# Performance work log

Hardware: AMD Instinct MI355X
Metric: run time of the kernel (lower is better)

Reference implementation:

```python
import jax, jax.numpy as jnp
import numpy as np

# ---- static configuration (matches init_kwargs) ----
B = 256              # graph pairs -> 2B graphs total (query/corpus interleaved)
N_PER_GRAPH = 24     # nodes per graph
N_MAX = 32           # max node set size (transport plan side)
E_PER_GRAPH = 200    # edges per graph
E_MAX = 256          # max_edge_set_size
D_EDGE = 256         # edge_feature_dim
D_SINK = 256         # sinkhorn_feature_dim
TEMPERATURE = 0.1
NUM_SINKHORN_ITERS = 20
NOISE_FACTOR = 0.0   # deterministic sinkhorn
CONSISTENCY_WEIGHT = 1.0


def setup_inputs() -> dict:
    rng = np.random.RandomState(0)
    num_graphs = 2 * B
    node_offset = np.arange(num_graphs) * N_PER_GRAPH
    graph_idx = np.repeat(np.arange(num_graphs), N_PER_GRAPH)
    # edges are grouped by graph (standard batched-graph layout)
    from_local = rng.randint(0, N_PER_GRAPH, size=(num_graphs, E_PER_GRAPH))
    to_local = rng.randint(0, N_PER_GRAPH, size=(num_graphs, E_PER_GRAPH))
    from_idx = (from_local + node_offset[:, None]).reshape(-1)
    to_idx = (to_local + node_offset[:, None]).reshape(-1)
    total_edges = num_graphs * E_PER_GRAPH

    key = jax.random.key(0)
    k = jax.random.split(key, 4)
    return {
        "edge_features_enc": jax.random.normal(k[0], (total_edges, D_EDGE), jnp.float32),
        "node_transport_plan": jax.random.uniform(k[1], (B, N_MAX, N_MAX), jnp.float32),
        "W1": jax.random.normal(k[2], (D_EDGE, D_SINK), jnp.float32) / np.sqrt(D_EDGE).astype(np.float32),
        "b1": jnp.zeros((D_SINK,), jnp.float32),
        "W2": jax.random.normal(k[3], (D_SINK, D_SINK), jnp.float32) / np.sqrt(D_SINK).astype(np.float32),
        "b2": jnp.zeros((D_SINK,), jnp.float32),
        "from_idx": jnp.asarray(from_idx, jnp.int32),
        "to_idx": jnp.asarray(to_idx, jnp.int32),
        "graph_idx": jnp.asarray(graph_idx, jnp.int32),
        "query_sizes": jnp.full((B,), N_PER_GRAPH, jnp.int32),
        "corpus_sizes": jnp.full((B,), N_PER_GRAPH, jnp.int32),
    }


def reference(edge_features_enc, node_transport_plan, W1, b1, W2, b2,
              from_idx, to_idx, graph_idx, query_sizes, corpus_sizes):
    num_graphs = 2 * B
    total_edges = from_idx.shape[0]

    # --- get_paired_edge_counts / split_and_stack ---
    g_edge = graph_idx[from_idx]                                   # graph id per edge
    edge_counts = jax.ops.segment_sum(jnp.ones_like(g_edge), g_edge, num_segments=num_graphs)
    edge_offset = jnp.cumsum(edge_counts) - edge_counts            # exclusive prefix
    rank = jnp.arange(total_edges, dtype=jnp.int32) - edge_offset[g_edge]

    stacked = jnp.zeros((num_graphs, E_MAX, D_EDGE), edge_features_enc.dtype)
    stacked = stacked.at[g_edge, rank].set(edge_features_enc)      # [2B, E_MAX, D]
    q_feat, c_feat = stacked[0::2], stacked[1::2]

    # --- sinkhorn_feature_layers (Linear-ReLU-Linear) + size mask ---
    def mlp(x):
        return jax.nn.relu(x @ W1 + b1) @ W2 + b2
    q_feat, c_feat = mlp(q_feat), mlp(c_feat)
    pos = jnp.arange(E_MAX)
    q_feat = q_feat * (pos[None, :] < query_sizes[:, None]).astype(q_feat.dtype)[..., None]
    c_feat = c_feat * (pos[None, :] < corpus_sizes[:, None]).astype(c_feat.dtype)[..., None]

    # --- kronecker_product_on_nodes: local endpoint ids, pad slots -> zero row N_MAX ---
    node_counts = jax.ops.segment_sum(jnp.ones_like(graph_idx), graph_idx, num_segments=num_graphs)
    node_offset = jnp.cumsum(node_counts) - node_counts
    pad = jnp.full((num_graphs, E_MAX), N_MAX, jnp.int32)
    f_loc = pad.at[g_edge, rank].set(from_idx - node_offset[g_edge])
    t_loc = pad.at[g_edge, rank].set(to_idx - node_offset[g_edge])
    fq, fc = f_loc[0::2], f_loc[1::2]
    tq, tc = t_loc[0::2], t_loc[1::2]

    T = jnp.pad(node_transport_plan, ((0, 0), (0, 1), (0, 1)))     # zero row/col for pads
    b = jnp.arange(B)[:, None, None]
    straight = T[b, fq[:, :, None], fc[:, None, :]] * T[b, tq[:, :, None], tc[:, None, :]]
    cross = T[b, fq[:, :, None], tc[:, None, :]] * T[b, tq[:, :, None], fc[:, None, :]]

    # --- sinkhorn_iters (log domain, noise_factor=0) ---
    log_alpha = (straight + cross) / TEMPERATURE                   # [B, E_MAX, E_MAX]
    def step(la, _):
        la = la - jax.nn.logsumexp(la, axis=2, keepdims=True)
        la = la - jax.nn.logsumexp(la, axis=1, keepdims=True)
        return la, None
    log_alpha, _ = jax.lax.scan(step, log_alpha, None, length=NUM_SINKHORN_ITERS)
    plan = jnp.exp(log_alpha)

    # --- feature_alignment_score: -sum(relu(q - P c)) per pair ---
    score = -jax.nn.relu(q_feat - plan @ c_feat).sum(axis=(1, 2))
    return CONSISTENCY_WEIGHT * score
```

## Files before the change

kernel.cpp:

```cpp
#include <hip/hip_runtime.h>

typedef unsigned short ushort_t;
typedef unsigned int uint_t;

typedef float f32x4_t __attribute__((ext_vector_type(4)));
typedef short s16x8_t __attribute__((ext_vector_type(8)));

#define NB   256
#define NG   512
#define NPG  24
#define NMAXI 32
#define EPG  200
#define DD   256
#define L2E_OVER_T 14.426950408889634f

__device__ __forceinline__ ushort_t f2bf(float f) {
    uint_t u = __float_as_uint(f);
    u += 0x7FFFu + ((u >> 16) & 1u);
    return (ushort_t)(u >> 16);
}
__device__ __forceinline__ float bfhi(uint_t u) { return __uint_as_float(u & 0xFFFF0000u); }
__device__ __forceinline__ float bflo(uint_t u) { return __uint_as_float(u << 16); }

__device__ __forceinline__ float frcp(float x) {
#if __has_builtin(__builtin_amdgcn_rcpf)
    return __builtin_amdgcn_rcpf(x);
#else
    return 1.0f / x;
#endif
}

__global__ __launch_bounds__(256) void prep_w(const float* __restrict__ W1,
                                              const float* __restrict__ W2,
                                              ushort_t* __restrict__ W1T,
                                              ushort_t* __restrict__ W2T)
{
    __shared__ float tile[2][4 * 256];
    const int t = threadIdx.x;
    const int k0 = blockIdx.x * 4;
    #pragma unroll
    for (int i = t; i < 4 * 256; i += 256) {
        tile[0][i] = W1[k0 * 256 + i];
        tile[1][i] = W2[k0 * 256 + i];
    }
    __syncthreads();
    const int n = t;
    #pragma unroll
    for (int m = 0; m < 2; ++m) {
        uint_t p0 = (uint_t)f2bf(tile[m][0 * 256 + n]) | ((uint_t)f2bf(tile[m][1 * 256 + n]) << 16);
        uint_t p1 = (uint_t)f2bf(tile[m][2 * 256 + n]) | ((uint_t)f2bf(tile[m][3 * 256 + n]) << 16);
        ushort_t* dst = (m ? W2T : W1T) + n * 256 + k0;
        uint2 pk; pk.x = p0; pk.y = p1;
        *(uint2*)dst = pk;
    }
}

__global__ __launch_bounds__(256) void mlp_kernel(
    const float* __restrict__ X, const ushort_t* __restrict__ W1T,
    const ushort_t* __restrict__ W2T, const float* __restrict__ b1,
    const float* __restrict__ b2, float* __restrict__ Y)
{
    __shared__ ushort_t sA[64 * 272];
    const int t = threadIdx.x;
    const int blk = blockIdx.x;
    const int lane = t & 63;
    const int w = t >> 6;
    const int quad = lane >> 4;
    const int mrow = lane & 15;

    {
        int r = t >> 2;
        int ch = (t & 3) * 64;
        int rho = blk * 64 + r;
        int g = rho / NPG;
        int e = rho - g * NPG;
        const float* src = X + ((size_t)(g * EPG + e)) * DD + ch;
        ushort_t* dst = &sA[r * 272 + ch];
        #pragma unroll
        for (int i = 0; i < 8; ++i) {
            float4 v0 = *(const float4*)(src + i * 8);
            float4 v1 = *(const float4*)(src + i * 8 + 4);
            uint4 pk;
            pk.x = (uint_t)f2bf(v0.x) | ((uint_t)f2bf(v0.y) << 16);
            pk.y = (uint_t)f2bf(v0.z) | ((uint_t)f2bf(v0.w) << 16);
            pk.z = (uint_t)f2bf(v1.x) | ((uint_t)f2bf(v1.y) << 16);
            pk.w = (uint_t)f2bf(v1.z) | ((uint_t)f2bf(v1.w) << 16);
            *(uint4*)(dst + i * 8) = pk;
        }
    }
    __syncthreads();

    f32x4_t acc[16];
    #pragma unroll
    for (int i = 0; i < 16; ++i) acc[i] = (f32x4_t){0.f, 0.f, 0.f, 0.f};

    #pragma unroll
    for (int k0 = 0; k0 < 256; k0 += 32) {
        s16x8_t a[4], bb[4];
        #pragma unroll
        for (int mt = 0; mt < 4; ++mt)
            a[mt] = *(const s16x8_t*)&sA[(mt * 16 + mrow) * 272 + k0 + quad * 8];
        #pragma unroll
        for (int nt = 0; nt < 4; ++nt)
            bb[nt] = *(const s16x8_t*)(W1T + (size_t)(64 * w + nt * 16 + mrow) * 256 + k0 + quad * 8);
        #pragma unroll
        for (int mt = 0; mt < 4; ++mt) {
            #pragma unroll
            for (int nt = 0; nt < 4; ++nt)
                acc[mt * 4 + nt] = __builtin_amdgcn_mfma_f32_16x16x32_bf16(
                    a[mt], bb[nt], acc[mt * 4 + nt], 0, 0, 0);
        }
    }
    __syncthreads();

    #pragma unroll
    for (int nt = 0; nt < 4; ++nt) {
        int col = 64 * w + nt * 16 + mrow;
        float bias = b1[col];
        #pragma unroll
        for (int mt = 0; mt < 4; ++mt) {
            f32x4_t v = acc[mt * 4 + nt];
            #pragma unroll
            for (int reg = 0; reg < 4; ++reg) {
                int row = mt * 16 + quad * 4 + reg;
                sA[row * 272 + col] = f2bf(fmaxf(v[reg] + bias, 0.f));
            }
        }
    }
    __syncthreads();

    #pragma unroll
    for (int i = 0; i < 16; ++i) acc[i] = (f32x4_t){0.f, 0.f, 0.f, 0.f};

    #pragma unroll
    for (int k0 = 0; k0 < 256; k0 += 32) {
        s16x8_t a[4], bb[4];
        #pragma unroll
        for (int mt = 0; mt < 4; ++mt)
            a[mt] = *(const s16x8_t*)&sA[(mt * 16 + mrow) * 272 + k0 + quad * 8];
        #pragma unroll
        for (int nt = 0; nt < 4; ++nt)
            bb[nt] = *(const s16x8_t*)(W2T + (size_t)(64 * w + nt * 16 + mrow) * 256 + k0 + quad * 8);
        #pragma unroll
        for (int mt = 0; mt < 4; ++mt) {
            #pragma unroll
            for (int nt = 0; nt < 4; ++nt)
                acc[mt * 4 + nt] = __builtin_amdgcn_mfma_f32_16x16x32_bf16(
                    a[mt], bb[nt], acc[mt * 4 + nt], 0, 0, 0);
        }
    }

    #pragma unroll
    for (int nt = 0; nt < 4; ++nt) {
        int col = 64 * w + nt * 16 + mrow;
        float bias = b2[col];
        #pragma unroll
        for (int mt = 0; mt < 4; ++mt) {
            f32x4_t v = acc[mt * 4 + nt];
            #pragma unroll
            for (int reg = 0; reg < 4; ++reg) {
                int row = blk * 64 + mt * 16 + quad * 4 + reg;
                Y[(size_t)row * 256 + col] = v[reg] + bias;
            }
        }
    }
}

__global__ __launch_bounds__(1024) void sink_kernel(
    const float* __restrict__ Tplan, const int* __restrict__ from_idx,
    const int* __restrict__ to_idx, const int* __restrict__ qsz,
    const int* __restrict__ csz, const float* __restrict__ qcf,
    float* __restrict__ out)
{
    const int b = blockIdx.x;
    const int t = threadIdx.x;
    const int R = t >> 4;
    const int C = t & 15;
    const int w = t >> 6;

    __shared__ __align__(16) char ovl[56320];
    __shared__ float ru_s[260];
    __shared__ float rv_p[320];
    __shared__ float wsum[16];

    float* Tl = (float*)ovl;
    int* fq = (int*)(ovl + 4368);
    int* tq = (int*)(ovl + 5392);
    int* fc = (int*)(ovl + 6416);
    int* tc = (int*)(ovl + 7440);
    float* Vp = (float*)ovl;
    float* plan_s = (float*)ovl;
    float* cf_s   = (float*)(ovl + 25600);

    for (int i = t; i < 33 * 33; i += 1024) Tl[i] = 0.f;
    if (t < 320) rv_p[t] = 1.0f;
    if (t < 256) {
        int gq = 2 * b, gc = 2 * b + 1;
        int a = NMAXI, bb = NMAXI, c = NMAXI, d = NMAXI;
        if (t < EPG) {
            a  = from_idx[gq * EPG + t] - gq * NPG;
            bb = to_idx  [gq * EPG + t] - gq * NPG;
            c  = from_idx[gc * EPG + t] - gc * NPG;
            d  = to_idx  [gc * EPG + t] - gc * NPG;
        }
        fq[t] = a; tq[t] = bb; fc[t] = c; tc[t] = d;
    }
    __syncthreads();
    {
        int i = t >> 5, j = t & 31;
        Tl[i * 33 + j] = Tplan[((size_t)b << 10) + t];
    }
    __syncthreads();

    uint_t Kp[4][8];
    {
        int fcl[16], tcl[16];
        #pragma unroll
        for (int o = 0; o < 16; ++o) { fcl[o] = fc[16 * C + o]; tcl[o] = tc[16 * C + o]; }
        #pragma unroll
        for (int i = 0; i < 4; ++i) {
            const float* T1 = &Tl[fq[4 * R + i] * 33];
            const float* T2 = &Tl[tq[4 * R + i] * 33];
            #pragma unroll
            for (int u = 0; u < 8; ++u) {
                int f0 = fcl[2 * u], t0 = tcl[2 * u];
                int f1 = fcl[2 * u + 1], t1 = tcl[2 * u + 1];
                float la0 = T1[f0] * T2[t0] + T1[t0] * T2[f0];
                float la1 = T1[f1] * T2[t1] + T1[t1] * T2[f1];
                Kp[i][u] = (uint_t)f2bf(exp2f(la0 * L2E_OVER_T))
                         | ((uint_t)f2bf(exp2f(la1 * L2E_OVER_T)) << 16);
            }
        }
    }

    for (int it = 0; it < 20; ++it) {
        {
            float4 rv0 = *(const float4*)&rv_p[20 * C + 0];
            float4 rv1 = *(const float4*)&rv_p[20 * C + 4];
            float4 rv2 = *(const float4*)&rv_p[20 * C + 8];
            float4 rv3 = *(const float4*)&rv_p[20 * C + 12];
            float pr[4];
            #pragma unroll
            for (int i = 0; i < 4; ++i) {
                float a0 = bflo(Kp[i][0]) * rv0.x + bfhi(Kp[i][0]) * rv0.y;
                float a1 = bflo(Kp[i][1]) * rv0.z + bfhi(Kp[i][1]) * rv0.w;
                float a2 = bflo(Kp[i][2]) * rv1.x + bfhi(Kp[i][2]) * rv1.y;
                float a3 = bflo(Kp[i][3]) * rv1.z + bfhi(Kp[i][3]) * rv1.w;
                a0 += bflo(Kp[i][4]) * rv2.x + bfhi(Kp[i][4]) * rv2.y;
                a1 += bflo(Kp[i][5]) * rv2.z + bfhi(Kp[i][5]) * rv2.w;
                a2 += bflo(Kp[i][6]) * rv3.x + bfhi(Kp[i][6]) * rv3.y;
                a3 += bflo(Kp[i][7]) * rv3.z + bfhi(Kp[i][7]) * rv3.w;
                pr[i] = (a0 + a1) + (a2 + a3);
            }
            #pragma unroll
            for (int i = 0; i < 4; ++i) {
                float s = pr[i];
                s += __shfl_xor(s, 1);
                s += __shfl_xor(s, 2);
                s += __shfl_xor(s, 4);
                s += __shfl_xor(s, 8);
                pr[i] = s;
            }
            if (C == 0) {
                #pragma unroll
                for (int i = 0; i < 4; ++i) ru_s[4 * R + i] = frcp(pr[i]);
            }
        }
        __syncthreads();
        {
            float u0 = ru_s[4 * R + 0], u1 = ru_s[4 * R + 1];
            float u2 = ru_s[4 * R + 2], u3 = ru_s[4 * R + 3];
            float pc[16];
            #pragma unroll
            for (int u = 0; u < 8; ++u) {
                float e0 = bflo(Kp[0][u]) * u0 + bflo(Kp[1][u]) * u1
                         + bflo(Kp[2][u]) * u2 + bflo(Kp[3][u]) * u3;
                float e1 = bfhi(Kp[0][u]) * u0 + bfhi(Kp[1][u]) * u1
                         + bfhi(Kp[2][u]) * u2 + bfhi(Kp[3][u]) * u3;
                pc[2 * u] = e0; pc[2 * u + 1] = e1;
            }
            #pragma unroll
            for (int k = 0; k < 16; ++k) {
                float s = pc[k];
                s += __shfl_xor(s, 16);
                s += __shfl_xor(s, 32);
                pc[k] = s;
            }
            if ((t & 63) < 16) {
                float* dst = &Vp[w * 272 + C * 16];
                *(float4*)(dst + 0)  = (float4){pc[0], pc[1], pc[2], pc[3]};
                *(float4*)(dst + 4)  = (float4){pc[4], pc[5], pc[6], pc[7]};
                *(float4*)(dst + 8)  = (float4){pc[8], pc[9], pc[10], pc[11]};
                *(float4*)(dst + 12) = (float4){pc[12], pc[13], pc[14], pc[15]};
            }
        }
        __syncthreads();
        if (t < 256) {
            float s = 0.f;
            #pragma unroll
            for (int ww = 0; ww < 16; ++ww) s += Vp[ww * 272 + t];
            rv_p[(t >> 4) * 20 + (t & 15)] = frcp(s);
        }
        __syncthreads();
    }

    int nq = qsz[b]; if (nq > 24) nq = 24;
    int nc = csz[b]; if (nc > 24) nc = 24;

    if (C < 2) {
        int umax = (C == 0) ? 8 : 4;
        #pragma unroll
        for (int i = 0; i < 4; ++i) {
            float rr = ru_s[4 * R + i];
            for (int u = 0; u < umax; ++u) {
                int j = 16 * C + 2 * u;
                plan_s[(4 * R + i) * 25 + j]     = bflo(Kp[i][u]) * rr * rv_p[20 * C + 2 * u];
                plan_s[(4 * R + i) * 25 + j + 1] = bfhi(Kp[i][u]) * rr * rv_p[20 * C + 2 * u + 1];
            }
        }
    }
    if (t < 768) {
        int j = t >> 5, inner = t & 31;
        int c = inner * 8;
        const float* src = qcf + ((size_t)(2 * b + 1) * 24 + j) * 256 + c;
        float4 v0 = *(const float4*)(src);
        float4 v1 = *(const float4*)(src + 4);
        float* dst = cf_s + j * 320 + (c >> 4) * 20 + (c & 15);
        *(float4*)dst = v0;
        *(float4*)(dst + 4) = v1;
    }
    __syncthreads();

    const int r0 = R * 4;
    const int m  = C;

    float pc[64];
    #pragma unroll
    for (int i = 0; i < 64; ++i) pc[i] = 0.f;

    for (int j = 0; j < nc; ++j) {
        float p0 = plan_s[(r0 + 0) * 25 + j];
        float p1 = plan_s[(r0 + 1) * 25 + j];
        float p2 = plan_s[(r0 + 2) * 25 + j];
        float p3 = plan_s[(r0 + 3) * 25 + j];
        const float4* cfp = (const float4*)(cf_s + j * 320 + m * 20);
        #pragma unroll
        for (int k = 0; k < 4; ++k) {
            float4 cv = cfp[k];
            pc[ 0 + k * 4 + 0] += p0 * cv.x; pc[ 0 + k * 4 + 1] += p0 * cv.y;
            pc[ 0 + k * 4 + 2] += p0 * cv.z; pc[ 0 + k * 4 + 3] += p0 * cv.w;
            pc[16 + k * 4 + 0] += p1 * cv.x; pc[16 + k * 4 + 1] += p1 * cv.y;
            pc[16 + k * 4 + 2] += p1 * cv.z; pc[16 + k * 4 + 3] += p1 * cv.w;
            pc[32 + k * 4 + 0] += p2 * cv.x; pc[32 + k * 4 + 1] += p2 * cv.y;
            pc[32 + k * 4 + 2] += p2 * cv.z; pc[32 + k * 4 + 3] += p2 * cv.w;
            pc[48 + k * 4 + 0] += p3 * cv.x; pc[48 + k * 4 + 1] += p3 * cv.y;
            pc[48 + k * 4 + 2] += p3 * cv.z; pc[48 + k * 4 + 3] += p3 * cv.w;
        }
    }

    float ssum = 0.f;
    const float* qbase = qcf + (size_t)(2 * b) * 24 * 256;
    #pragma unroll
    for (int i = 0; i < 4; ++i) {
        int row = r0 + i;
        if (row < nq) {
            const float4* qp = (const float4*)(qbase + (size_t)row * 256 + m * 16);
            #pragma unroll
            for (int k = 0; k < 4; ++k) {
                float4 qv = qp[k];
                ssum += fmaxf(qv.x - pc[i * 16 + k * 4 + 0], 0.f);
                ssum += fmaxf(qv.y - pc[i * 16 + k * 4 + 1], 0.f);
                ssum += fmaxf(qv.z - pc[i * 16 + k * 4 + 2], 0.f);
                ssum += fmaxf(qv.w - pc[i * 16 + k * 4 + 3], 0.f);
            }
        } else {
            #pragma unroll
            for (int k = 0; k < 16; ++k) ssum += fmaxf(-pc[i * 16 + k], 0.f);
        }
    }
    ssum += __shfl_xor(ssum, 1);
    ssum += __shfl_xor(ssum, 2);
    ssum += __shfl_xor(ssum, 4);
    ssum += __shfl_xor(ssum, 8);
    ssum += __shfl_xor(ssum, 16);
    ssum += __shfl_xor(ssum, 32);
    if ((t & 63) == 0) wsum[t >> 6] = ssum;
    __syncthreads();
    if (t == 0) {
        float s = 0.f;
        #pragma unroll
        for (int i = 0; i < 16; ++i) s += wsum[i];
        out[b] = -s;
    }
}

extern "C" void kernel_launch(void* const* d_in, const int* in_sizes, int n_in,
                              void* d_out, int out_size, void* d_ws, size_t ws_size,
                              hipStream_t stream)
{
    const float* edge_feat = (const float*)d_in[0];
    const float* tplan     = (const float*)d_in[1];
    const float* W1        = (const float*)d_in[2];
    const float* b1        = (const float*)d_in[3];
    const float* W2        = (const float*)d_in[4];
    const float* b2        = (const float*)d_in[5];
    const int*   from_idx  = (const int*)d_in[6];
    const int*   to_idx    = (const int*)d_in[7];
    const int*   qsz       = (const int*)d_in[9];
    const int*   csz       = (const int*)d_in[10];
    float* out = (float*)d_out;

    char* ws = (char*)d_ws;
    ushort_t* W1T = (ushort_t*)ws;
    ushort_t* W2T = W1T + 65536;
    float* qcf = (float*)(ws + 262144);

    prep_w<<<64, 256, 0, stream>>>(W1, W2, W1T, W2T);
    mlp_kernel<<<192, 256, 0, stream>>>(edge_feat, W1T, W2T, b1, b2, qcf);
    sink_kernel<<<256, 1024, 0, stream>>>(tplan, from_idx, to_idx, qsz, csz, qcf, out);
}
```

Baseline: 266.5 us.

## Shrink MLP tiles, drop sinkhorn row-scale barrier, read corpus features from global

```diff
diff --git a/kernel.cpp b/kernel.cpp
--- a/kernel.cpp
+++ b/kernel.cpp
@@ -28,6 +28,14 @@
 #else
     return 1.0f / x;
 #endif
+}
+
+__device__ __forceinline__ float red16(float s) {
+    s += __shfl_xor(s, 1);
+    s += __shfl_xor(s, 2);
+    s += __shfl_xor(s, 4);
+    s += __shfl_xor(s, 8);
+    return s;
 }
 
 __global__ __launch_bounds__(256) void prep_w(const float* __restrict__ W1,
@@ -60,7 +68,7 @@
     const ushort_t* __restrict__ W2T, const float* __restrict__ b1,
     const float* __restrict__ b2, float* __restrict__ Y)
 {
-    __shared__ ushort_t sA[64 * 272];
+    __shared__ ushort_t sA[16 * 272];
     const int t = threadIdx.x;
     const int blk = blockIdx.x;
     const int lane = t & 63;
@@ -69,15 +77,15 @@
     const int mrow = lane & 15;
 
     {
-        int r = t >> 2;
-        int ch = (t & 3) * 64;
-        int rho = blk * 64 + r;
+        int r = t >> 4;
+        int ch = (t & 15) * 16;
+        int rho = blk * 16 + r;
         int g = rho / NPG;
         int e = rho - g * NPG;
         const float* src = X + ((size_t)(g * EPG + e)) * DD + ch;
         ushort_t* dst = &sA[r * 272 + ch];
         #pragma unroll
-        for (int i = 0; i < 8; ++i) {
+        for (int i = 0; i < 2; ++i) {
             float4 v0 = *(const float4*)(src + i * 8);
             float4 v1 = *(const float4*)(src + i * 8 + 4);
             uint4 pk;
@@ -90,25 +98,17 @@
     }
     __syncthreads();
 
-    f32x4_t acc[16];
-    #pragma unroll
-    for (int i = 0; i < 16; ++i) acc[i] = (f32x4_t){0.f, 0.f, 0.f, 0.f};
+    f32x4_t acc[4];
+    #pragma unroll
+    for (int i = 0; i < 4; ++i) acc[i] = (f32x4_t){0.f, 0.f, 0.f, 0.f};
 
     #pragma unroll
     for (int k0 = 0; k0 < 256; k0 += 32) {
-        s16x8_t a[4], bb[4];
-        #pragma unroll
-        for (int mt = 0; mt < 4; ++mt)
-            a[mt] = *(const s16x8_t*)&sA[(mt * 16 + mrow) * 272 + k0 + quad * 8];
-        #pragma unroll
-        for (int nt = 0; nt < 4; ++nt)
-            bb[nt] = *(const s16x8_t*)(W1T + (size_t)(64 * w + nt * 16 + mrow) * 256 + k0 + quad * 8);
-        #pragma unroll
-        for (int mt = 0; mt < 4; ++mt) {
-            #pragma unroll
-            for (int nt = 0; nt < 4; ++nt)
-                acc[mt * 4 + nt] = __builtin_amdgcn_mfma_f32_16x16x32_bf16(
-                    a[mt], bb[nt], acc[mt * 4 + nt], 0, 0, 0);
+        s16x8_t a = *(const s16x8_t*)&sA[mrow * 272 + k0 + quad * 8];
+        #pragma unroll
+        for (int nt = 0; nt < 4; ++nt) {
+            s16x8_t bb = *(const s16x8_t*)(W1T + (size_t)(64 * w + nt * 16 + mrow) * 256 + k0 + quad * 8);
+            acc[nt] = __builtin_amdgcn_mfma_f32_16x16x32_bf16(a, bb, acc[nt], 0, 0, 0);
         }
     }
     __syncthreads();
@@ -117,36 +117,25 @@
     for (int nt = 0; nt < 4; ++nt) {
         int col = 64 * w + nt * 16 + mrow;
         float bias = b1[col];
-        #pragma unroll
-        for (int mt = 0; mt < 4; ++mt) {
-            f32x4_t v = acc[mt * 4 + nt];
-            #pragma unroll
-            for (int reg = 0; reg < 4; ++reg) {
-                int row = mt * 16 + quad * 4 + reg;
-                sA[row * 272 + col] = f2bf(fmaxf(v[reg] + bias, 0.f));
-            }
-        }
-    }
-    __syncthreads();
-
-    #pragma unroll
-    for (int i = 0; i < 16; ++i) acc[i] = (f32x4_t){0.f, 0.f, 0.f, 0.f};
+        f32x4_t v = acc[nt];
+        #pragma unroll
+        for (int reg = 0; reg < 4; ++reg) {
+            int row = quad * 4 + reg;
+            sA[row * 272 + col] = f2bf(fmaxf(v[reg] + bias, 0.f));
+        }
+    }
+    __syncthreads();
+
+    #pragma unroll
+    for (int i = 0; i < 4; ++i) acc[i] = (f32x4_t){0.f, 0.f, 0.f, 0.f};
 
     #pragma unroll
     for (int k0 = 0; k0 < 256; k0 += 32) {
-        s16x8_t a[4], bb[4];
-        #pragma unroll
-        for (int mt = 0; mt < 4; ++mt)
-            a[mt] = *(const s16x8_t*)&sA[(mt * 16 + mrow) * 272 + k0 + quad * 8];
-        #pragma unroll
-        for (int nt = 0; nt < 4; ++nt)
-            bb[nt] = *(const s16x8_t*)(W2T + (size_t)(64 * w + nt * 16 + mrow) * 256 + k0 + quad * 8);
-        #pragma unroll
-        for (int mt = 0; mt < 4; ++mt) {
-            #pragma unroll
-            for (int nt = 0; nt < 4; ++nt)
-                acc[mt * 4 + nt] = __builtin_amdgcn_mfma_f32_16x16x32_bf16(
-                    a[mt], bb[nt], acc[mt * 4 + nt], 0, 0, 0);
+        s16x8_t a = *(const s16x8_t*)&sA[mrow * 272 + k0 + quad * 8];
+        #pragma unroll
+        for (int nt = 0; nt < 4; ++nt) {
+            s16x8_t bb = *(const s16x8_t*)(W2T + (size_t)(64 * w + nt * 16 + mrow) * 256 + k0 + quad * 8);
+            acc[nt] = __builtin_amdgcn_mfma_f32_16x16x32_bf16(a, bb, acc[nt], 0, 0, 0);
         }
     }
 
@@ -154,14 +143,11 @@
     for (int nt = 0; nt < 4; ++nt) {
         int col = 64 * w + nt * 16 + mrow;
         float bias = b2[col];
-        #pragma unroll
-        for (int mt = 0; mt < 4; ++mt) {
-            f32x4_t v = acc[mt * 4 + nt];
-            #pragma unroll
-            for (int reg = 0; reg < 4; ++reg) {
-                int row = blk * 64 + mt * 16 + quad * 4 + reg;
-                Y[(size_t)row * 256 + col] = v[reg] + bias;
-            }
+        f32x4_t v = acc[nt];
+        #pragma unroll
+        for (int reg = 0; reg < 4; ++reg) {
+            int row = blk * 16 + quad * 4 + reg;
+            Y[(size_t)row * 256 + col] = v[reg] + bias;
         }
     }
 }
@@ -178,8 +164,7 @@
     const int C = t & 15;
     const int w = t >> 6;
 
-    __shared__ __align__(16) char ovl[56320];
-    __shared__ float ru_s[260];
+    __shared__ __align__(16) char ovl[25600];
     __shared__ float rv_p[320];
     __shared__ float wsum[16];
 
@@ -190,7 +175,6 @@
     int* tc = (int*)(ovl + 7440);
     float* Vp = (float*)ovl;
     float* plan_s = (float*)ovl;
-    float* cf_s   = (float*)(ovl + 25600);
 
     for (int i = t; i < 33 * 33; i += 1024) Tl[i] = 0.f;
     if (t < 320) rv_p[t] = 1.0f;
@@ -233,13 +217,13 @@
         }
     }
 
+    float u_r[4];
     for (int it = 0; it < 20; ++it) {
         {
             float4 rv0 = *(const float4*)&rv_p[20 * C + 0];
             float4 rv1 = *(const float4*)&rv_p[20 * C + 4];
             float4 rv2 = *(const float4*)&rv_p[20 * C + 8];
             float4 rv3 = *(const float4*)&rv_p[20 * C + 12];
-            float pr[4];
             #pragma unroll
             for (int i = 0; i < 4; ++i) {
                 float a0 = bflo(Kp[i][0]) * rv0.x + bfhi(Kp[i][0]) * rv0.y;
@@ -250,26 +234,13 @@
                 a1 += bflo(Kp[i][5]) * rv2.z + bfhi(Kp[i][5]) * rv2.w;
                 a2 += bflo(Kp[i][6]) * rv3.x + bfhi(Kp[i][6]) * rv3.y;
                 a3 += bflo(Kp[i][7]) * rv3.z + bfhi(Kp[i][7]) * rv3.w;
-                pr[i] = (a0 + a1) + (a2 + a3);
-            }
-            #pragma unroll
-            for (int i = 0; i < 4; ++i) {
-                float s = pr[i];
-                s += __shfl_xor(s, 1);
-                s += __shfl_xor(s, 2);
-                s += __shfl_xor(s, 4);
-                s += __shfl_xor(s, 8);
-                pr[i] = s;
-            }
-            if (C == 0) {
-                #pragma unroll
-                for (int i = 0; i < 4; ++i) ru_s[4 * R + i] = frcp(pr[i]);
-            }
-        }
-        __syncthreads();
+                float s = (a0 + a1) + (a2 + a3);
+                s = red16(s);
+                u_r[i] = frcp(s);
+            }
+        }
         {
-            float u0 = ru_s[4 * R + 0], u1 = ru_s[4 * R + 1];
-            float u2 = ru_s[4 * R + 2], u3 = ru_s[4 * R + 3];
+            float u0 = u_r[0], u1 = u_r[1], u2 = u_r[2], u3 = u_r[3];
             float pc[16];
             #pragma unroll
             for (int u = 0; u < 8; ++u) {
@@ -311,7 +282,7 @@
         int umax = (C == 0) ? 8 : 4;
         #pragma unroll
         for (int i = 0; i < 4; ++i) {
-            float rr = ru_s[4 * R + i];
+            float rr = u_r[i];
             for (int u = 0; u < umax; ++u) {
                 int j = 16 * C + 2 * u;
                 plan_s[(4 * R + i) * 25 + j]     = bflo(Kp[i][u]) * rr * rv_p[20 * C + 2 * u];
@@ -319,42 +290,33 @@
             }
         }
     }
-    if (t < 768) {
-        int j = t >> 5, inner = t & 31;
-        int c = inner * 8;
-        const float* src = qcf + ((size_t)(2 * b + 1) * 24 + j) * 256 + c;
-        float4 v0 = *(const float4*)(src);
-        float4 v1 = *(const float4*)(src + 4);
-        float* dst = cf_s + j * 320 + (c >> 4) * 20 + (c & 15);
-        *(float4*)dst = v0;
-        *(float4*)(dst + 4) = v1;
-    }
     __syncthreads();
 
     const int r0 = R * 4;
     const int m  = C;
 
-    float pc[64];
-    #pragma unroll
-    for (int i = 0; i < 64; ++i) pc[i] = 0.f;
-
+    float ps[64];
+    #pragma unroll
+    for (int i = 0; i < 64; ++i) ps[i] = 0.f;
+
+    const float* cfb = qcf + (size_t)(2 * b + 1) * 24 * 256 + m * 16;
     for (int j = 0; j < nc; ++j) {
         float p0 = plan_s[(r0 + 0) * 25 + j];
         float p1 = plan_s[(r0 + 1) * 25 + j];
         float p2 = plan_s[(r0 + 2) * 25 + j];
         float p3 = plan_s[(r0 + 3) * 25 + j];
-        const float4* cfp = (const float4*)(cf_s + j * 320 + m * 20);
+        const float4* cfp = (const float4*)(cfb + (size_t)j * 256);
         #pragma unroll
         for (int k = 0; k < 4; ++k) {
             float4 cv = cfp[k];
-            pc[ 0 + k * 4 + 0] += p0 * cv.x; pc[ 0 + k * 4 + 1] += p0 * cv.y;
-            pc[ 0 + k * 4 + 2] += p0 * cv.z; pc[ 0 + k * 4 + 3] += p0 * cv.w;
-            pc[16 + k * 4 + 0] += p1 * cv.x; pc[16 + k * 4 + 1] += p1 * cv.y;
-            pc[16 + k * 4 + 2] += p1 * cv.z; pc[16 + k * 4 + 3] += p1 * cv.w;
-            pc[32 + k * 4 + 0] += p2 * cv.x; pc[32 + k * 4 + 1] += p2 * cv.y;
-            pc[32 + k * 4 + 2] += p2 * cv.z; pc[32 + k * 4 + 3] += p2 * cv.w;
-            pc[48 + k * 4 + 0] += p3 * cv.x; pc[48 + k * 4 + 1] += p3 * cv.y;
-            pc[48 + k * 4 + 2] += p3 * cv.z; pc[48 + k * 4 + 3] += p3 * cv.w;
+            ps[ 0 + k * 4 + 0] += p0 * cv.x; ps[ 0 + k * 4 + 1] += p0 * cv.y;
+            ps[ 0 + k * 4 + 2] += p0 * cv.z; ps[ 0 + k * 4 + 3] += p0 * cv.w;
+            ps[16 + k * 4 + 0] += p1 * cv.x; ps[16 + k * 4 + 1] += p1 * cv.y;
+            ps[16 + k * 4 + 2] += p1 * cv.z; ps[16 + k * 4 + 3] += p1 * cv.w;
+            ps[32 + k * 4 + 0] += p2 * cv.x; ps[32 + k * 4 + 1] += p2 * cv.y;
+            ps[32 + k * 4 + 2] += p2 * cv.z; ps[32 + k * 4 + 3] += p2 * cv.w;
+            ps[48 + k * 4 + 0] += p3 * cv.x; ps[48 + k * 4 + 1] += p3 * cv.y;
+            ps[48 + k * 4 + 2] += p3 * cv.z; ps[48 + k * 4 + 3] += p3 * cv.w;
         }
     }
 
@@ -368,14 +330,14 @@
             #pragma unroll
             for (int k = 0; k < 4; ++k) {
                 float4 qv = qp[k];
-                ssum += fmaxf(qv.x - pc[i * 16 + k * 4 + 0], 0.f);
-                ssum += fmaxf(qv.y - pc[i * 16 + k * 4 + 1], 0.f);
-                ssum += fmaxf(qv.z - pc[i * 16 + k * 4 + 2], 0.f);
-                ssum += fmaxf(qv.w - pc[i * 16 + k * 4 + 3], 0.f);
+                ssum += fmaxf(qv.x - ps[i * 16 + k * 4 + 0], 0.f);
+                ssum += fmaxf(qv.y - ps[i * 16 + k * 4 + 1], 0.f);
+                ssum += fmaxf(qv.z - ps[i * 16 + k * 4 + 2], 0.f);
+                ssum += fmaxf(qv.w - ps[i * 16 + k * 4 + 3], 0.f);
             }
         } else {
             #pragma unroll
-            for (int k = 0; k < 16; ++k) ssum += fmaxf(-pc[i * 16 + k], 0.f);
+            for (int k = 0; k < 16; ++k) ssum += fmaxf(-ps[i * 16 + k], 0.f);
         }
     }
     ssum += __shfl_xor(ssum, 1);
@@ -416,6 +378,6 @@
     float* qcf = (float*)(ws + 262144);
 
     prep_w<<<64, 256, 0, stream>>>(W1, W2, W1T, W2T);
-    mlp_kernel<<<192, 256, 0, stream>>>(edge_feat, W1T, W2T, b1, b2, qcf);
+    mlp_kernel<<<768, 256, 0, stream>>>(edge_feat, W1T, W2T, b1, b2, qcf);
     sink_kernel<<<256, 1024, 0, stream>>>(tplan, from_idx, to_idx, qsz, csz, qcf, out);
 }
```

Result: slower. 408.4 us (+53.3%).
